# Kernel tuning notes

Hardware: AMD Instinct MI355X
Metric: run time of the kernel (lower is better)

The kernel has to match this reference:

```python
import jax, jax.numpy as jnp
import numpy as np

B, N, D, H = 2, 2048, 768, 12
HD = D // H  # head_dim = 64
SCALE = HD ** -0.5


def setup_inputs() -> dict:
    key = jax.random.key(0)
    ks = jax.random.split(key, 8)
    return {
        "x": jax.random.normal(ks[0], (B, N, D), jnp.float32),
        "masks": jax.random.uniform(ks[1], (B, H, N), jnp.float32),
        "lambda_r": jax.random.uniform(ks[2], (B, H), jnp.float32) * 4.0 + 1.0,
        "theta_r": jax.random.uniform(ks[3], (B, H), jnp.float32),
        "mask_weights": jax.random.uniform(ks[4], (B, H), jnp.float32),
        "qkv_w": jax.random.normal(ks[5], (D, 3 * D), jnp.float32) * (D ** -0.5),
        "qkv_b": jnp.zeros((3 * D,), jnp.float32),
        "proj_w": jax.random.normal(ks[6], (D, D), jnp.float32) * (D ** -0.5),
        "proj_b": jnp.zeros((D,), jnp.float32),
    }


def reference(x, masks, lambda_r, theta_r, mask_weights, qkv_w, qkv_b, proj_w, proj_b):
    # qkv projection: [B,N,3D] -> [3,B,H,N,HD]
    qkv = (x @ qkv_w + qkv_b).reshape(B, N, 3, H, HD).transpose(2, 0, 3, 1, 4)
    q, k, v = qkv[0], qkv[1], qkv[2]
    # raw scores [B,H,N,N]
    attn = jnp.einsum('bhqd,bhkd->bhqk', q, k) * SCALE
    # region gate: sigmoid(lambda * (m_i*m_j - theta)) multiplied into scores pre-softmax
    gate = jax.nn.sigmoid(
        lambda_r[:, :, None, None]
        * (masks[:, :, :, None] * masks[:, :, None, :] - theta_r[:, :, None, None])
    )
    attn = jax.nn.softmax(attn * gate, axis=-1)  # dropout is identity in eval
    out = jnp.einsum('bhqk,bhkd->bqhd', attn, v).reshape(B, N, D)
    # per-head output scaling via mask_weights
    out = out * jnp.repeat(mask_weights, HD, axis=-1)[:, None, :]
    return out @ proj_w + proj_b
```

## Files before the change

### kernel.cpp

```cpp
#include <hip/hip_runtime.h>

typedef unsigned short u16;
typedef unsigned int u32;
typedef __attribute__((ext_vector_type(8))) short short8;
typedef __attribute__((ext_vector_type(4))) float f32x4;

#define NB 2
#define NSEQ 2048
#define DIM 768
#define NH 12
#define HDIM 64

#if defined(__has_builtin)
#if __has_builtin(__builtin_amdgcn_exp2f)
#define EXPB(x) __builtin_amdgcn_exp2f(x)
#define CFOLD 0.18033688f
#define HAVE_EXP2 1
#endif
#if __has_builtin(__builtin_amdgcn_fractf)
#define FRACT(x) __builtin_amdgcn_fractf(x)
#endif
#endif
#ifndef HAVE_EXP2
#define EXPB(x) __expf(x)
#define CFOLD 0.125f
#endif
#ifndef FRACT
#define FRACT(x) ((x) - floorf(x))
#endif

__device__ __forceinline__ u16 f2bf(float x) {
    union { float f; unsigned u; } v; v.f = x;
    unsigned r = v.u + 0x7fffu + ((v.u >> 16) & 1u);
    return (u16)(r >> 16);
}

__device__ __forceinline__ u32 pack_bf16(float a, float b) {
    union { float f; u32 u; } A, B; A.f = a; B.f = b;
    u32 ra = A.u + 0x7fffu + ((A.u >> 16) & 1u);
    u32 rb = B.u + 0x7fffu + ((B.u >> 16) & 1u);
    return __builtin_amdgcn_perm(rb, ra, 0x07060302u);
}

__device__ __forceinline__ f32x4 mfma16(short8 a, short8 b, f32x4 c) {
    return __builtin_amdgcn_mfma_f32_16x16x32_bf16(a, b, c, 0, 0, 0);
}

__device__ __forceinline__ void glds16(const u16* g, u16* l) {
    __builtin_amdgcn_global_load_lds((const __attribute__((address_space(1))) u32*)g,
                                     (__attribute__((address_space(3))) u32*)l, 16, 0, 0);
}


__global__ __launch_bounds__(256) void convert_x(const float* __restrict__ in,
                                                 u16* __restrict__ outp) {
    int i = (blockIdx.x * 256 + threadIdx.x) * 4;
    float4 v = *(const float4*)(in + i);
    *(uint2*)(outp + i) = make_uint2(pack_bf16(v.x, v.y), pack_bf16(v.z, v.w));
}

__global__ __launch_bounds__(256) void transpose_to_bf16(const float* __restrict__ in,
                                                         u16* __restrict__ outp,
                                                         int rows, int cols) {
    __shared__ float tile[32][33];
    int c0 = blockIdx.x * 32, r0 = blockIdx.y * 32;
    int tx = threadIdx.x & 31, ty = threadIdx.x >> 5;
    #pragma unroll
    for (int i = 0; i < 32; i += 8)
        tile[ty + i][tx] = in[(size_t)(r0 + ty + i) * cols + c0 + tx];
    __syncthreads();
    #pragma unroll
    for (int i = 0; i < 32; i += 8)
        outp[(size_t)(c0 + ty + i) * rows + r0 + tx] = f2bf(tile[tx][ty + i]);
}

__global__ __launch_bounds__(256) void vtrans(const u16* __restrict__ vin,
                                              u16* __restrict__ vout) {
    __shared__ __align__(16) u16 tile[64][72];
    const int bh = blockIdx.y;
    const int n0 = blockIdx.x * 64;
    const int t = threadIdx.x;
    const size_t base = (size_t)bh * NSEQ * HDIM;
    int r = t >> 3, cb = (t & 7) * 8;
    *(uint4*)&tile[r][cb]      = *(const uint4*)&vin[base + (size_t)(n0 + r) * HDIM + cb];
    *(uint4*)&tile[r + 32][cb] = *(const uint4*)&vin[base + (size_t)(n0 + r + 32) * HDIM + cb];
    __syncthreads();
    #pragma unroll
    for (int half = 0; half < 2; half++) {
        int d = (t >> 3) + half * 32;
        int nb = (t & 7) * 8;
        short8 v;
        #pragma unroll
        for (int j = 0; j < 8; j++) v[j] = (short)tile[nb + j][d];
        *(short8*)&vout[base + (size_t)d * NSEQ + n0 + nb] = v;
    }
}

__global__ __launch_bounds__(256) void gemm_qkv(const u16* __restrict__ A,
                                                const u16* __restrict__ BT,
                                                const float* __restrict__ bias,
                                                u16* __restrict__ qo,
                                                u16* __restrict__ ko,
                                                u16* __restrict__ vo) {
    __shared__ __align__(16) u16 As[128 * 32];
    __shared__ __align__(16) u16 Bs[128 * 32];
    const int bm = blockIdx.y * 128, bn = blockIdx.x * 128;
    const int t = threadIdx.x;
    const int lane = t & 63, wave = t >> 6;
    const int l15 = lane & 15, quad = lane >> 4;
    const int wm = (wave >> 1) * 64, wn = (wave & 1) * 64;

    const u16* ga = A + (size_t)(bm + (t >> 2)) * DIM + (t & 3) * 8;
    const u16* gb = BT + (size_t)(bn + (t >> 2)) * DIM + (t & 3) * 8;
    u16* la = As + wave * 512;
    u16* lb = Bs + wave * 512;

    f32x4 acc[4][4] = {};
    for (int k0 = 0; k0 < DIM; k0 += 32) {
        __syncthreads();
        glds16(ga, la);
        glds16(ga + (size_t)64 * DIM, la + 2048);
        glds16(gb, lb);
        glds16(gb + (size_t)64 * DIM, lb + 2048);
        ga += 32; gb += 32;
        __syncthreads();
        short8 af[4], bf[4];
        #pragma unroll
        for (int i = 0; i < 4; i++) af[i] = *(const short8*)&As[(wm + i * 16 + l15) * 32 + quad * 8];
        #pragma unroll
        for (int j = 0; j < 4; j++) bf[j] = *(const short8*)&Bs[(wn + j * 16 + l15) * 32 + quad * 8];
        #pragma unroll
        for (int i = 0; i < 4; i++)
            #pragma unroll
            for (int j = 0; j < 4; j++)
                acc[i][j] = mfma16(af[i], bf[j], acc[i][j]);
    }

    #pragma unroll
    for (int i = 0; i < 4; i++) {
        int mr = bm + wm + i * 16 + quad * 4;
        int b = mr >> 11, nn = mr & 2047;
        #pragma unroll
        for (int j = 0; j < 4; j++) {
            int ncol = bn + wn + j * 16 + l15;
            int w = ncol / DIM, rem = ncol - w * DIM;
            int h = rem >> 6, hd = rem & 63;
            u16* dst = (w == 0) ? qo : (w == 1) ? ko : vo;
            float bb = bias[ncol];
            size_t idx = (((size_t)(b * NH + h)) * NSEQ + nn) * HDIM + hd;
            #pragma unroll
            for (int r = 0; r < 4; r++)
                dst[idx + (size_t)r * HDIM] = f2bf(acc[i][j][r] + bb);
        }
    }
}

__global__ __launch_bounds__(256) void attn_kernel(const u16* __restrict__ Q,
                                                   const u16* __restrict__ Kg,
                                                   const u16* __restrict__ Vt,
                                                   const float* __restrict__ masks,
                                                   const float* __restrict__ lambda_r,
                                                   const float* __restrict__ theta_r,
                                                   const float* __restrict__ mask_w,
                                                   u16* __restrict__ AO) {
    const int bh = blockIdx.y;
    const int b = bh / NH, h = bh % NH;
    const int qb = blockIdx.x * 64;
    const int t = threadIdx.x, wave = t >> 6, lane = t & 63;
    const int l15 = lane & 15, quad = lane >> 4;

    __shared__ __align__(16) u16 Ks[64 * 64];
    __shared__ __align__(16) u16 Vs[64 * 64];
    __shared__ __align__(16) u16 Ps[4][16 * 72];
    __shared__ __align__(16) float mks[64];
    __shared__ float gt[1026];
    __shared__ __align__(8) float2 ptab[1025];

    const float lam = lambda_r[bh], th = theta_r[bh], mw = mask_w[bh];

    for (int i = t; i < 1026; i += 256) {
        float u = i * (1.0f / 1024.0f);
        float z = lam * (u - th);
        gt[i] = (1.0f / (1.0f + __expf(-z))) * CFOLD;
    }
    __syncthreads();
    for (int i = t; i < 1025; i += 256) {
        float a = gt[i];
        ptab[i] = make_float2(a, gt[i + 1] - a);
    }

    const size_t base = (size_t)bh * (NSEQ * HDIM);
    const int qrow = qb + wave * 16;

    const u16* Qr = Q + base + (size_t)(qrow + l15) * HDIM;
    short8 bq0 = *(const short8*)(Qr + quad * 8);
    short8 bq1 = *(const short8*)(Qr + 32 + quad * 8);
    const float mq1024 = masks[bh * NSEQ + qrow + l15] * 1024.0f;

    const int srow = t >> 3, scb = t & 7;
    const int gcb = scb ^ (srow & 7);
    const u16* kgp = Kg + base + (size_t)srow * HDIM + gcb * 8;
    const u16* vgp = Vt + base + (size_t)srow * NSEQ + gcb * 8;
    u16* ksl = Ks + wave * 512;
    u16* vsl = Vs + wave * 512;

    const int ph = (quad ^ (l15 & 7)) * 8;
    const int kb0 = l15 * 64 + ph, kb1 = l15 * 64 + (ph ^ 32);
    u16* PsW = Ps[wave];
    const int pw = l15 * 72 + quad * 4;
    const int prd = l15 * 72 + quad * 8;

    float ls0 = 0.f, ls1 = 0.f, ls2 = 0.f, ls3 = 0.f;
    f32x4 O[4] = {};

    for (int kt = 0; kt < NSEQ / 64; kt++) {
        __syncthreads();
        glds16(kgp, ksl);
        glds16(kgp + 2048, ksl + 2048);
        glds16(vgp, vsl);
        glds16(vgp + (size_t)32 * NSEQ, vsl + 2048);
        if (t < 16) *(float4*)&mks[t * 4] = *(const float4*)&masks[bh * NSEQ + kt * 64 + t * 4];
        kgp += 4096; vgp += 64;
        __syncthreads();

        #pragma unroll
        for (int c = 0; c < 4; c++) {
            short8 ak0 = *(const short8*)&Ks[kb0 + c * 1024];
            short8 ak1 = *(const short8*)&Ks[kb1 + c * 1024];
            f32x4 S = {0.f, 0.f, 0.f, 0.f};
            S = mfma16(ak0, bq0, S);
            S = mfma16(ak1, bq1, S);
            float4 mkv = *(const float4*)&mks[c * 16 + quad * 4];
            float p[4];
            #pragma unroll
            for (int r = 0; r < 4; r++) {
                float mk = (r == 0) ? mkv.x : (r == 1) ? mkv.y : (r == 2) ? mkv.z : mkv.w;
                float xf = mq1024 * mk;
                int i = (int)xf;
                float fr = FRACT(xf);
                float2 pe = ptab[i];
                float gp = fmaf(fr, pe.y, pe.x);
                p[r] = EXPB(S[r] * gp);
            }
            ls0 += p[0]; ls1 += p[1]; ls2 += p[2]; ls3 += p[3];
            *(uint2*)&PsW[pw + c * 16] = make_uint2(pack_bf16(p[0], p[1]), pack_bf16(p[2], p[3]));
        }

        #pragma unroll
        for (int kc = 0; kc < 2; kc++) {
            short8 bp = *(const short8*)&PsW[prd + kc * 32];
            const int vb = (kc == 0) ? kb0 : kb1;
            #pragma unroll
            for (int dt = 0; dt < 4; dt++) {
                short8 av = *(const short8*)&Vs[vb + dt * 1024];
                O[dt] = mfma16(av, bp, O[dt]);
            }
        }
    }

    float lsum = (ls0 + ls1) + (ls2 + ls3);
    lsum += __shfl_xor(lsum, 16);
    lsum += __shfl_xor(lsum, 32);
    float sc = mw / lsum;

    u16* aor = AO + ((size_t)(b * NSEQ) + qrow + l15) * DIM + h * HDIM + quad * 4;
    #pragma unroll
    for (int dt = 0; dt < 4; dt++) {
        *(uint2*)(aor + dt * 16) = make_uint2(pack_bf16(O[dt][0] * sc, O[dt][1] * sc),
                                              pack_bf16(O[dt][2] * sc, O[dt][3] * sc));
    }
}

__global__ __launch_bounds__(256) void gemm_proj(const u16* __restrict__ A,
                                                 const u16* __restrict__ BT,
                                                 const float* __restrict__ bias,
                                                 float* __restrict__ outp) {
    __shared__ __align__(16) u16 As[128 * 32];
    __shared__ __align__(16) u16 Bs[64 * 32];
    const int bm = blockIdx.y * 128, bn = blockIdx.x * 64;
    const int t = threadIdx.x;
    const int lane = t & 63, wave = t >> 6;
    const int l15 = lane & 15, quad = lane >> 4;
    const int wm = wave * 32;

    const u16* ga = A + (size_t)(bm + (t >> 2)) * DIM + (t & 3) * 8;
    const u16* gb = BT + (size_t)(bn + (t >> 2)) * DIM + (t & 3) * 8;
    u16* la = As + wave * 512;
    u16* lb = Bs + wave * 512;

    f32x4 acc[2][4] = {};
    for (int k0 = 0; k0 < DIM; k0 += 32) {
        __syncthreads();
        glds16(ga, la);
        glds16(ga + (size_t)64 * DIM, la + 2048);
        glds16(gb, lb);
        ga += 32; gb += 32;
        __syncthreads();
        short8 af[2], bf[4];
        #pragma unroll
        for (int i = 0; i < 2; i++) af[i] = *(const short8*)&As[(wm + i * 16 + l15) * 32 + quad * 8];
        #pragma unroll
        for (int j = 0; j < 4; j++) bf[j] = *(const short8*)&Bs[(j * 16 + l15) * 32 + quad * 8];
        #pragma unroll
        for (int i = 0; i < 2; i++)
            #pragma unroll
            for (int j = 0; j < 4; j++)
                acc[i][j] = mfma16(af[i], bf[j], acc[i][j]);
    }

    #pragma unroll
    for (int i = 0; i < 2; i++) {
        int mr = bm + wm + i * 16 + quad * 4;
        #pragma unroll
        for (int j = 0; j < 4; j++) {
            int ncol = bn + j * 16 + l15;
            float bb = bias[ncol];
            #pragma unroll
            for (int r = 0; r < 4; r++)
                outp[(size_t)(mr + r) * DIM + ncol] = acc[i][j][r] + bb;
        }
    }
}

extern "C" void kernel_launch(void* const* d_in, const int* in_sizes, int n_in,
                              void* d_out, int out_size, void* d_ws, size_t ws_size,
                              hipStream_t stream) {
    const float* x            = (const float*)d_in[0];
    const float* masks        = (const float*)d_in[1];
    const float* lambda_r     = (const float*)d_in[2];
    const float* theta_r      = (const float*)d_in[3];
    const float* mask_weights = (const float*)d_in[4];
    const float* qkv_w        = (const float*)d_in[5];
    const float* qkv_b        = (const float*)d_in[6];
    const float* proj_w       = (const float*)d_in[7];
    const float* proj_b       = (const float*)d_in[8];
    float* outp = (float*)d_out;

    const size_t SZH = (size_t)NB * NH * NSEQ * HDIM;
    u16* xb    = (u16*)d_ws;
    u16* wqkvT = xb + (size_t)4096 * 768;
    u16* wprT  = wqkvT + (size_t)2304 * 768;
    u16* qg    = wprT + (size_t)768 * 768;
    u16* kg    = qg + SZH;
    u16* vtmp  = kg + SZH;
    u16* vt    = vtmp + SZH;
    u16* ao    = xb;

    convert_x<<<dim3((4096 * 768) / (4 * 256)), 256, 0, stream>>>(x, xb);
    transpose_to_bf16<<<dim3(2304 / 32, 768 / 32), 256, 0, stream>>>(qkv_w, wqkvT, 768, 2304);
    transpose_to_bf16<<<dim3(768 / 32, 768 / 32), 256, 0, stream>>>(proj_w, wprT, 768, 768);
    gemm_qkv<<<dim3(2304 / 128, 4096 / 128), 256, 0, stream>>>(xb, wqkvT, qkv_b, qg, kg, vtmp);
    vtrans<<<dim3(NSEQ / 64, NB * NH), 256, 0, stream>>>(vtmp, vt);
    attn_kernel<<<dim3(NSEQ / 64, NB * NH), 256, 0, stream>>>(qg, kg, vt, masks, lambda_r,
                                                              theta_r, mask_weights, ao);
    gemm_proj<<<dim3(768 / 64, 4096 / 128), 256, 0, stream>>>(ao, wprT, proj_b, outp);
}
```

Baseline: 197.3 us.

## Merge prep kernels, compute gate analytically, give each attention wave two query tiles

The three preprocessing launches (x conversion and two weight transposes) become one prep kernel that dispatches by block index, removing launch overhead. The attention kernel drops the per-block sigmoid lookup table and its interpolation and computes the gate directly with exp2 and a fast reciprocal. Blocks shrink to 128 threads, and each wave now handles 32 query rows (two 16-row groups), so every K/V fragment read from LDS feeds twice as many MFMAs. The cost is more transcendental operations per score and more registers per wave.

```diff
diff --git a/kernel.cpp b/kernel.cpp
--- a/kernel.cpp
+++ b/kernel.cpp
@@ -11,22 +11,23 @@
 #define NH 12
 #define HDIM 64
 
+#define LOG2E 1.44269504088896f
+#define CFOLD 0.18033688f
+
 #if defined(__has_builtin)
 #if __has_builtin(__builtin_amdgcn_exp2f)
 #define EXPB(x) __builtin_amdgcn_exp2f(x)
-#define CFOLD 0.18033688f
-#define HAVE_EXP2 1
+#else
+#define EXPB(x) exp2f(x)
 #endif
-#if __has_builtin(__builtin_amdgcn_fractf)
-#define FRACT(x) __builtin_amdgcn_fractf(x)
+#if __has_builtin(__builtin_amdgcn_rcpf)
+#define RCP(x) __builtin_amdgcn_rcpf(x)
+#else
+#define RCP(x) (1.0f / (x))
 #endif
-#endif
-#ifndef HAVE_EXP2
-#define EXPB(x) __expf(x)
-#define CFOLD 0.125f
-#endif
-#ifndef FRACT
-#define FRACT(x) ((x) - floorf(x))
+#else
+#define EXPB(x) exp2f(x)
+#define RCP(x) (1.0f / (x))
 #endif
 
 __device__ __forceinline__ u16 f2bf(float x) {
@@ -51,20 +52,28 @@
                                      (__attribute__((address_space(3))) u32*)l, 16, 0, 0);
 }
 
-
-__global__ __launch_bounds__(256) void convert_x(const float* __restrict__ in,
-                                                 u16* __restrict__ outp) {
-    int i = (blockIdx.x * 256 + threadIdx.x) * 4;
-    float4 v = *(const float4*)(in + i);
-    *(uint2*)(outp + i) = make_uint2(pack_bf16(v.x, v.y), pack_bf16(v.z, v.w));
-}
-
-__global__ __launch_bounds__(256) void transpose_to_bf16(const float* __restrict__ in,
-                                                         u16* __restrict__ outp,
-                                                         int rows, int cols) {
+__global__ __launch_bounds__(256) void prep(const float* __restrict__ x, u16* __restrict__ xb,
+                                            const float* __restrict__ qkv_w, u16* __restrict__ wq,
+                                            const float* __restrict__ proj_w, u16* __restrict__ wp) {
+    const int t = threadIdx.x;
+    int bid = blockIdx.x;
+    if (bid < 3072) {
+        int i = (bid * 256 + t) * 4;
+        float4 v = *(const float4*)(x + i);
+        *(uint2*)(xb + i) = make_uint2(pack_bf16(v.x, v.y), pack_bf16(v.z, v.w));
+        return;
+    }
+    const float* in; u16* outp; int rows, cols, bx, by;
+    if (bid < 3072 + 1728) {
+        bid -= 3072; in = qkv_w; outp = wq; rows = 768; cols = 2304;
+        bx = bid % 72; by = bid / 72;
+    } else {
+        bid -= 4800; in = proj_w; outp = wp; rows = 768; cols = 768;
+        bx = bid % 24; by = bid / 24;
+    }
     __shared__ float tile[32][33];
-    int c0 = blockIdx.x * 32, r0 = blockIdx.y * 32;
-    int tx = threadIdx.x & 31, ty = threadIdx.x >> 5;
+    int c0 = bx * 32, r0 = by * 32;
+    int tx = t & 31, ty = t >> 5;
     #pragma unroll
     for (int i = 0; i < 32; i += 8)
         tile[ty + i][tx] = in[(size_t)(r0 + ty + i) * cols + c0 + tx];
@@ -155,7 +164,7 @@
     }
 }
 
-__global__ __launch_bounds__(256) void attn_kernel(const u16* __restrict__ Q,
+__global__ __launch_bounds__(128) void attn_kernel(const u16* __restrict__ Q,
                                                    const u16* __restrict__ Kg,
                                                    const u16* __restrict__ Vt,
                                                    const float* __restrict__ masks,
@@ -171,31 +180,27 @@
 
     __shared__ __align__(16) u16 Ks[64 * 64];
     __shared__ __align__(16) u16 Vs[64 * 64];
-    __shared__ __align__(16) u16 Ps[4][16 * 72];
+    __shared__ __align__(16) u16 Ps[2][2304];
     __shared__ __align__(16) float mks[64];
-    __shared__ float gt[1026];
-    __shared__ __align__(8) float2 ptab[1025];
 
     const float lam = lambda_r[bh], th = theta_r[bh], mw = mask_w[bh];
-
-    for (int i = t; i < 1026; i += 256) {
-        float u = i * (1.0f / 1024.0f);
-        float z = lam * (u - th);
-        gt[i] = (1.0f / (1.0f + __expf(-z))) * CFOLD;
-    }
-    __syncthreads();
-    for (int i = t; i < 1025; i += 256) {
-        float a = gt[i];
-        ptab[i] = make_float2(a, gt[i + 1] - a);
-    }
+    const float Bfac = lam * th * LOG2E;
 
     const size_t base = (size_t)bh * (NSEQ * HDIM);
-    const int qrow = qb + wave * 16;
-
-    const u16* Qr = Q + base + (size_t)(qrow + l15) * HDIM;
-    short8 bq0 = *(const short8*)(Qr + quad * 8);
-    short8 bq1 = *(const short8*)(Qr + 32 + quad * 8);
-    const float mq1024 = masks[bh * NSEQ + qrow + l15] * 1024.0f;
+    const int qrow = qb + wave * 32;
+
+    short8 bq[2][2];
+    float Afac[2], lsum[2];
+    #pragma unroll
+    for (int g = 0; g < 2; g++) {
+        const u16* Qr = Q + base + (size_t)(qrow + g * 16 + l15) * HDIM;
+        bq[g][0] = *(const short8*)(Qr + quad * 8);
+        bq[g][1] = *(const short8*)(Qr + 32 + quad * 8);
+        float mq = masks[bh * NSEQ + qrow + g * 16 + l15];
+        Afac[g] = -lam * LOG2E * mq;
+        lsum[g] = 0.f;
+    }
+    f32x4 O[2][4] = {};
 
     const int srow = t >> 3, scb = t & 7;
     const int gcb = scb ^ (srow & 7);
@@ -210,64 +215,68 @@
     const int pw = l15 * 72 + quad * 4;
     const int prd = l15 * 72 + quad * 8;
 
-    float ls0 = 0.f, ls1 = 0.f, ls2 = 0.f, ls3 = 0.f;
-    f32x4 O[4] = {};
+    const float* mrow = masks + bh * NSEQ;
 
     for (int kt = 0; kt < NSEQ / 64; kt++) {
         __syncthreads();
-        glds16(kgp, ksl);
-        glds16(kgp + 2048, ksl + 2048);
-        glds16(vgp, vsl);
-        glds16(vgp + (size_t)32 * NSEQ, vsl + 2048);
-        if (t < 16) *(float4*)&mks[t * 4] = *(const float4*)&masks[bh * NSEQ + kt * 64 + t * 4];
-        kgp += 4096; vgp += 64;
+        #pragma unroll
+        for (int i = 0; i < 4; i++) glds16(kgp + i * 16 * HDIM, ksl + i * 1024);
+        #pragma unroll
+        for (int i = 0; i < 4; i++) glds16(vgp + (size_t)i * 16 * NSEQ, vsl + i * 1024);
+        if (t < 16) *(float4*)&mks[t * 4] = *(const float4*)&mrow[kt * 64 + t * 4];
+        kgp += 64 * HDIM; vgp += 64;
         __syncthreads();
 
         #pragma unroll
         for (int c = 0; c < 4; c++) {
             short8 ak0 = *(const short8*)&Ks[kb0 + c * 1024];
             short8 ak1 = *(const short8*)&Ks[kb1 + c * 1024];
-            f32x4 S = {0.f, 0.f, 0.f, 0.f};
-            S = mfma16(ak0, bq0, S);
-            S = mfma16(ak1, bq1, S);
             float4 mkv = *(const float4*)&mks[c * 16 + quad * 4];
-            float p[4];
-            #pragma unroll
-            for (int r = 0; r < 4; r++) {
-                float mk = (r == 0) ? mkv.x : (r == 1) ? mkv.y : (r == 2) ? mkv.z : mkv.w;
-                float xf = mq1024 * mk;
-                int i = (int)xf;
-                float fr = FRACT(xf);
-                float2 pe = ptab[i];
-                float gp = fmaf(fr, pe.y, pe.x);
-                p[r] = EXPB(S[r] * gp);
+            #pragma unroll
+            for (int g = 0; g < 2; g++) {
+                f32x4 S = {0.f, 0.f, 0.f, 0.f};
+                S = mfma16(ak0, bq[g][0], S);
+                S = mfma16(ak1, bq[g][1], S);
+                float p[4];
+                #pragma unroll
+                for (int r = 0; r < 4; r++) {
+                    float mk = (r == 0) ? mkv.x : (r == 1) ? mkv.y : (r == 2) ? mkv.z : mkv.w;
+                    float e = EXPB(fmaf(mk, Afac[g], Bfac));
+                    float gate = RCP(1.0f + e);
+                    p[r] = EXPB(S[r] * CFOLD * gate);
+                }
+                lsum[g] += (p[0] + p[1]) + (p[2] + p[3]);
+                *(uint2*)&PsW[g * 1152 + pw + c * 16] =
+                    make_uint2(pack_bf16(p[0], p[1]), pack_bf16(p[2], p[3]));
             }
-            ls0 += p[0]; ls1 += p[1]; ls2 += p[2]; ls3 += p[3];
-            *(uint2*)&PsW[pw + c * 16] = make_uint2(pack_bf16(p[0], p[1]), pack_bf16(p[2], p[3]));
         }
 
         #pragma unroll
         for (int kc = 0; kc < 2; kc++) {
-            short8 bp = *(const short8*)&PsW[prd + kc * 32];
-            const int vb = (kc == 0) ? kb0 : kb1;
+            const int vb = kc ? kb1 : kb0;
+            short8 bp0 = *(const short8*)&PsW[prd + kc * 32];
+            short8 bp1 = *(const short8*)&PsW[1152 + prd + kc * 32];
             #pragma unroll
             for (int dt = 0; dt < 4; dt++) {
                 short8 av = *(const short8*)&Vs[vb + dt * 1024];
-                O[dt] = mfma16(av, bp, O[dt]);
+                O[0][dt] = mfma16(av, bp0, O[0][dt]);
+                O[1][dt] = mfma16(av, bp1, O[1][dt]);
             }
         }
     }
 
-    float lsum = (ls0 + ls1) + (ls2 + ls3);
-    lsum += __shfl_xor(lsum, 16);
-    lsum += __shfl_xor(lsum, 32);
-    float sc = mw / lsum;
-
-    u16* aor = AO + ((size_t)(b * NSEQ) + qrow + l15) * DIM + h * HDIM + quad * 4;
-    #pragma unroll
-    for (int dt = 0; dt < 4; dt++) {
-        *(uint2*)(aor + dt * 16) = make_uint2(pack_bf16(O[dt][0] * sc, O[dt][1] * sc),
-                                              pack_bf16(O[dt][2] * sc, O[dt][3] * sc));
+    #pragma unroll
+    for (int g = 0; g < 2; g++) {
+        float ls = lsum[g];
+        ls += __shfl_xor(ls, 16);
+        ls += __shfl_xor(ls, 32);
+        float sc = mw / ls;
+        u16* aor = AO + ((size_t)(b * NSEQ) + qrow + g * 16 + l15) * DIM + h * HDIM + quad * 4;
+        #pragma unroll
+        for (int dt = 0; dt < 4; dt++) {
+            *(uint2*)(aor + dt * 16) = make_uint2(pack_bf16(O[g][dt][0] * sc, O[g][dt][1] * sc),
+                                                  pack_bf16(O[g][dt][2] * sc, O[g][dt][3] * sc));
+        }
     }
 }
 
@@ -346,12 +355,10 @@
     u16* vt    = vtmp + SZH;
     u16* ao    = xb;
 
-    convert_x<<<dim3((4096 * 768) / (4 * 256)), 256, 0, stream>>>(x, xb);
-    transpose_to_bf16<<<dim3(2304 / 32, 768 / 32), 256, 0, stream>>>(qkv_w, wqkvT, 768, 2304);
-    transpose_to_bf16<<<dim3(768 / 32, 768 / 32), 256, 0, stream>>>(proj_w, wprT, 768, 768);
+    prep<<<dim3(3072 + 1728 + 576), 256, 0, stream>>>(x, xb, qkv_w, wqkvT, proj_w, wprT);
     gemm_qkv<<<dim3(2304 / 128, 4096 / 128), 256, 0, stream>>>(xb, wqkvT, qkv_b, qg, kg, vtmp);
     vtrans<<<dim3(NSEQ / 64, NB * NH), 256, 0, stream>>>(vtmp, vt);
-    attn_kernel<<<dim3(NSEQ / 64, NB * NH), 256, 0, stream>>>(qg, kg, vt, masks, lambda_r,
+    attn_kernel<<<dim3(NSEQ / 64, NB * NH), 128, 0, stream>>>(qg, kg, vt, masks, lambda_r,
                                                               theta_r, mask_weights, ao);
     gemm_proj<<<dim3(768 / 64, 4096 / 128), 256, 0, stream>>>(ao, wprT, proj_b, outp);
 }
```

Result: slower. 218.9 us (+10.9%).
